# Performance work log

Measured on AMD Instinct MI355X. Metric: run time of the kernel, lower is better.

Reference implementation:

```python
import jax, jax.numpy as jnp
import numpy as np

EPS = 1e-5

def _lc(x, w, b, stride, pad):
    # x: [B,H,W]; w: [Ho,Wo,kh,kw]; b: [Ho,Wo]
    Ho, Wo, kh, kw = w.shape
    patches = jax.lax.conv_general_dilated_patches(
        x[:, None], (kh, kw), (stride, stride), [(pad, pad), (pad, pad)])
    # patches: [B, kh*kw, Ho, Wo]
    out = jnp.einsum('bkij,ijk->bij', patches, w.reshape(Ho, Wo, kh * kw))
    return out + b

def _ln2d(x, g, b):
    # torch LayerNorm over the last two (spatial) dims
    mu = x.mean(axis=(1, 2), keepdims=True)
    var = ((x - mu) ** 2).mean(axis=(1, 2), keepdims=True)
    return (x - mu) * jax.lax.rsqrt(var + EPS) * g + b

def _pool(x):
    # MaxPool2d(kernel=2, stride=2) over spatial dims of [B,H,W]
    return jax.lax.reduce_window(x, -jnp.inf, jax.lax.max, (1, 2, 2), (1, 2, 2), 'VALID')

def setup_inputs() -> dict:
    key = jax.random.key(0)
    ks = jax.random.split(key, 32)
    d = {}
    d['x'] = jax.random.normal(ks[0], (64, 128, 128), jnp.float32)
    sizes = [(128, 7), (64, 5), (64, 5), (32, 3), (32, 3), (16, 3)]
    for i, (s, k) in enumerate(sizes, start=1):
        d[f'w{i}'] = jax.random.normal(ks[4 * i], (s, s, k, k), jnp.float32) / k
        d[f'b{i}'] = jax.random.normal(ks[4 * i + 1], (s, s), jnp.float32)
        d[f'g{i}'] = jnp.ones((s, s), jnp.float32)
        d[f'be{i}'] = jnp.zeros((s, s), jnp.float32)
    d['fcw'] = jax.random.normal(ks[30], (1024, 256), jnp.float32) / np.sqrt(256.0)
    d['fcb'] = jax.random.normal(ks[31], (1024,), jnp.float32) * 0.01
    return d

def reference(x, w1, b1, g1, be1, w2, b2, g2, be2, w3, b3, g3, be3,
              w4, b4, g4, be4, w5, b5, g5, be5, w6, b6, g6, be6, fcw, fcb):
    # dropout is identity (eval / p=0)
    h = _pool(_ln2d(jax.nn.relu(_lc(x, w1, b1, 1, 3)), g1, be1))   # [B,64,64]
    h = _ln2d(jax.nn.relu(_lc(h, w2, b2, 1, 2)), g2, be2)          # [B,64,64]
    h = _pool(_ln2d(jax.nn.relu(_lc(h, w3, b3, 1, 2)), g3, be3))   # [B,32,32]
    h = _ln2d(jax.nn.relu(_lc(h, w4, b4, 1, 1)), g4, be4)          # [B,32,32]
    h = _pool(_ln2d(jax.nn.relu(_lc(h, w5, b5, 1, 1)), g5, be5))   # [B,16,16]
    h = _ln2d(jax.nn.relu(_lc(h, w6, b6, 1, 1)), g6, be6)          # [B,16,16]
    h = h.reshape(h.shape[0], -1) @ fcw.T + fcb                    # [B,1024]
    return jax.nn.softmax(h, axis=-1)
```

## Files before the change

### kernel.cpp

```cpp
#include <hip/hip_runtime.h>

#define LN_EPS 1e-5f

constexpr int T1_OFF   = 0;
constexpr int WT2_OFF  = 1048576;
constexpr int WT3_OFF  = WT2_OFF + 102400;
constexpr int WT4_OFF  = WT3_OFF + 102400;
constexpr int WT5_OFF  = WT4_OFF + 9216;
constexpr int WT6_OFF  = WT5_OFF + 9216;
constexpr int FCWT_OFF = WT6_OFF + 2304;

constexpr int NREP = 136;

__global__ __launch_bounds__(256) void s1_conv(const float* __restrict__ x,
                                               const float* __restrict__ w1,
                                               const float* __restrict__ b1,
                                               const float* __restrict__ w2,
                                               const float* __restrict__ w3,
                                               const float* __restrict__ w4,
                                               const float* __restrict__ w5,
                                               const float* __restrict__ w6,
                                               const float* __restrict__ fcw,
                                               float* __restrict__ ws)
{
    const int tid = threadIdx.x;

    if (blockIdx.x < NREP) {
        const int rb = blockIdx.x;
        if (rb < 32) {
            for (int idx = rb * 256 + tid; idx < 102400; idx += 32 * 256) {
                int p = idx / 25, k = idx % 25;
                ws[WT2_OFF + k * 4096 + p] = w2[idx];
            }
        } else if (rb < 64) {
            for (int idx = (rb - 32) * 256 + tid; idx < 102400; idx += 32 * 256) {
                int p = idx / 25, k = idx % 25;
                ws[WT3_OFF + k * 4096 + p] = w3[idx];
            }
        } else if (rb < 68) {
            for (int idx = (rb - 64) * 256 + tid; idx < 9216; idx += 4 * 256) {
                int p = idx / 9, k = idx % 9;
                ws[WT4_OFF + k * 1024 + p] = w4[idx];
            }
        } else if (rb < 72) {
            for (int idx = (rb - 68) * 256 + tid; idx < 9216; idx += 4 * 256) {
                int p = idx / 9, k = idx % 9;
                ws[WT5_OFF + k * 1024 + p] = w5[idx];
            }
        } else if (rb < 73) {
            for (int idx = tid; idx < 2304; idx += 256) {
                int p = idx / 9, k = idx % 9;
                ws[WT6_OFF + k * 256 + p] = w6[idx];
            }
        } else {
            for (int idx = (rb - 73) * 256 + tid; idx < 262144; idx += 63 * 256) {
                int r = idx >> 8, kc = idx & 255;
                int kq = kc >> 2, c = kc & 3;
                ws[FCWT_OFF + kq * 4096 + r * 4 + c] = fcw[idx];
            }
        }
        return;
    }

    constexpr int R = 128, K = 7, TILE = 8, S = 16, PAD = 3;
    constexpr int RT = TILE + K - 1;
    constexpr int PP = RT * RT + 1;
    constexpr int NBLK = R / TILE;
    constexpr int WCNT = TILE * TILE * K * K;
    constexpr int PG = 256 / S;
    constexpr int OPT = TILE * TILE / PG;

    __shared__ float s_in[S * PP];
    __shared__ float s_w[WCNT];
    __shared__ float s_b[TILE * TILE];

    float* t1 = ws + T1_OFF;
    const int cb = blockIdx.x - NREP;
    const int bt = cb % (NBLK * NBLK);
    const int sg = cb / (NBLK * NBLK);
    const int i0 = (bt / NBLK) * TILE;
    const int j0 = (bt % NBLK) * TILE;
    const int S0 = sg * S;

    for (int idx = tid; idx < WCNT; idx += 256) {
        int pi = idx / (K * K), kk = idx % (K * K);
        int gi = i0 + pi / TILE, gj = j0 + pi % TILE;
        s_w[idx] = w1[(gi * R + gj) * (K * K) + kk];
    }
    if (tid < TILE * TILE)
        s_b[tid] = b1[(i0 + tid / TILE) * R + (j0 + tid % TILE)];

    for (int idx = tid; idx < S * RT * RT; idx += 256) {
        int ls = idx / (RT * RT), p = idx % (RT * RT);
        int ci = i0 - PAD + p / RT, cj = j0 - PAD + p % RT;
        float v = 0.0f;
        if (ci >= 0 && ci < R && cj >= 0 && cj < R)
            v = x[(S0 + ls) * R * R + ci * R + cj];
        s_in[ls * PP + p] = v;
    }
    __syncthreads();

    const int s = tid % S;
    const int pg = tid / S;
    const int p0 = pg * OPT;
    const int ti = p0 / TILE, tj0 = p0 % TILE;
    float acc[OPT];
    #pragma unroll
    for (int o = 0; o < OPT; o++) acc[o] = s_b[p0 + o];
    #pragma unroll
    for (int ki = 0; ki < K; ki++) {
        float row[OPT + K - 1];
        #pragma unroll
        for (int c = 0; c < OPT + K - 1; c++)
            row[c] = s_in[s * PP + (ti + ki) * RT + tj0 + c];
        #pragma unroll
        for (int kj = 0; kj < K; kj++)
            #pragma unroll
            for (int o = 0; o < OPT; o++)
                acc[o] += row[o + kj] * s_w[(p0 + o) * (K * K) + ki * K + kj];
    }
    #pragma unroll
    for (int o = 0; o < OPT; o++)
        t1[(S0 + s) * R * R + (i0 + ti) * R + (j0 + tj0 + o)] = fmaxf(acc[o], 0.0f);
}

constexpr int NT = 1024;
constexpr int NW = NT / 64;

__device__ __forceinline__ void stats_reduce(float* red, float lsum, float lsq,
                                             float inv_n, float* s_mu, float* s_rs)
{
    const int tid = threadIdx.x;
    #pragma unroll
    for (int off = 32; off > 0; off >>= 1) {
        lsum += __shfl_down(lsum, off, 64);
        lsq  += __shfl_down(lsq,  off, 64);
    }
    if ((tid & 63) == 0) { red[tid >> 6] = lsum; red[NW + (tid >> 6)] = lsq; }
    __syncthreads();
    if (tid == 0) {
        float a = 0.f, b = 0.f;
        #pragma unroll
        for (int i = 0; i < NW; i++) { a += red[i]; b += red[NW + i]; }
        float mu = a * inv_n, ms = b * inv_n;
        *s_mu = mu;
        *s_rs = rsqrtf(ms - mu * mu + LN_EPS);
    }
    __syncthreads();
}

template<int M, int K>
__device__ __forceinline__ void conv_lds(const float* __restrict__ I,
                                         const float* __restrict__ wT,
                                         const float* __restrict__ bias,
                                         float* __restrict__ R,
                                         float& lsum, float& lsq)
{
    constexpr int NPOS = M * M;
    constexpr int PADK = (K - 1) / 2;
    constexpr int STR = M + 1;
    constexpr int OPT = (NPOS + NT - 1) / NT;
    const int tid = threadIdx.x;

    #pragma unroll
    for (int o = 0; o < OPT; o++) {
        int p = tid + o * NT;
        if (NPOS < NT && p >= NPOS) break;
        int i = p / M, j = p % M;
        float acc = bias[p];
        #pragma unroll
        for (int ki = 0; ki < K; ki++) {
            int ii = i - PADK + ki;
            bool rok = (ii >= 0 && ii < M);
            #pragma unroll
            for (int kj = 0; kj < K; kj++) {
                int jj = j - PADK + kj;
                float iv = (rok && jj >= 0 && jj < M) ? I[ii * STR + jj] : 0.0f;
                acc += iv * wT[(ki * K + kj) * NPOS + p];
            }
        }
        float v = fmaxf(acc, 0.0f);
        R[i * STR + j] = v;
        lsum += v;
        lsq  += v * v;
    }
}

template<int N, bool POOL>
__device__ __forceinline__ void transform(const float* __restrict__ R,
                                          float mu, float rs,
                                          const float* __restrict__ g,
                                          const float* __restrict__ b,
                                          float* __restrict__ I)
{
    constexpr int M = POOL ? N / 2 : N;
    constexpr int SR = N + 1, SI = M + 1;
    const int tid = threadIdx.x;
    for (int p = tid; p < M * M; p += NT) {
        int i = p / M, j = p % M;
        float v;
        if constexpr (POOL) {
            float best = -3.4e38f;
            #pragma unroll
            for (int dy = 0; dy < 2; dy++)
                #pragma unroll
                for (int dx = 0; dx < 2; dx++) {
                    int r = 2 * i + dy, c = 2 * j + dx;
                    float n = (R[r * SR + c] - mu) * rs * g[r * N + c] + b[r * N + c];
                    best = fmaxf(best, n);
                }
            v = best;
        } else {
            v = (R[i * SR + j] - mu) * rs * g[i * N + j] + b[i * N + j];
        }
        I[i * SI + j] = v;
    }
}

__global__ __launch_bounds__(1024) void tail_fused(
    const float* __restrict__ ws_ro,
    const float* __restrict__ g1, const float* __restrict__ be1,
    const float* __restrict__ b2,
    const float* __restrict__ g2, const float* __restrict__ be2,
    const float* __restrict__ b3,
    const float* __restrict__ g3, const float* __restrict__ be3,
    const float* __restrict__ b4,
    const float* __restrict__ g4, const float* __restrict__ be4,
    const float* __restrict__ b5,
    const float* __restrict__ g5, const float* __restrict__ be5,
    const float* __restrict__ b6,
    const float* __restrict__ g6, const float* __restrict__ be6,
    const float* __restrict__ fcb,
    float* __restrict__ outp)
{
    __shared__ __align__(16) float I[64 * 65];
    __shared__ __align__(16) float R[64 * 65];
    __shared__ __align__(16) float h[256];
    __shared__ float red[2 * NW];
    __shared__ float s_mu, s_rs;

    const int s = blockIdx.x;
    const int tid = threadIdx.x;
    const float* x1  = ws_ro + T1_OFF + s * 16384;
    const float* wT2 = ws_ro + WT2_OFF;
    const float* wT3 = ws_ro + WT3_OFF;
    const float* wT4 = ws_ro + WT4_OFF;
    const float* wT5 = ws_ro + WT5_OFF;
    const float* wT6 = ws_ro + WT6_OFF;

    float ls = 0.f, lq = 0.f;
    {
        const float4* x4 = (const float4*)x1;
        #pragma unroll
        for (int i = tid; i < 4096; i += NT) {
            float4 v = x4[i];
            ls += v.x + v.y + v.z + v.w;
            lq += v.x * v.x + v.y * v.y + v.z * v.z + v.w * v.w;
        }
    }
    stats_reduce(red, ls, lq, 1.f / 16384.f, &s_mu, &s_rs);

    {
        float mu = s_mu, rs = s_rs;
        #pragma unroll
        for (int o = 0; o < 4; o++) {
            int p = tid + o * NT;
            int i = p >> 6, j = p & 63;
            float2 xa = *((const float2*)(x1 + (2 * i) * 128 + 2 * j));
            float2 xb = *((const float2*)(x1 + (2 * i + 1) * 128 + 2 * j));
            float2 ga = *((const float2*)(g1 + (2 * i) * 128 + 2 * j));
            float2 gb = *((const float2*)(g1 + (2 * i + 1) * 128 + 2 * j));
            float2 ba = *((const float2*)(be1 + (2 * i) * 128 + 2 * j));
            float2 bb = *((const float2*)(be1 + (2 * i + 1) * 128 + 2 * j));
            float n0 = (xa.x - mu) * rs * ga.x + ba.x;
            float n1 = (xa.y - mu) * rs * ga.y + ba.y;
            float n2 = (xb.x - mu) * rs * gb.x + bb.x;
            float n3 = (xb.y - mu) * rs * gb.y + bb.y;
            I[i * 65 + j] = fmaxf(fmaxf(n0, n1), fmaxf(n2, n3));
        }
    }
    __syncthreads();

    ls = lq = 0.f; conv_lds<64, 5>(I, wT2, b2, R, ls, lq);
    stats_reduce(red, ls, lq, 1.f / 4096.f, &s_mu, &s_rs);
    transform<64, false>(R, s_mu, s_rs, g2, be2, I);
    __syncthreads();

    ls = lq = 0.f; conv_lds<64, 5>(I, wT3, b3, R, ls, lq);
    stats_reduce(red, ls, lq, 1.f / 4096.f, &s_mu, &s_rs);
    transform<64, true>(R, s_mu, s_rs, g3, be3, I);
    __syncthreads();

    ls = lq = 0.f; conv_lds<32, 3>(I, wT4, b4, R, ls, lq);
    stats_reduce(red, ls, lq, 1.f / 1024.f, &s_mu, &s_rs);
    transform<32, false>(R, s_mu, s_rs, g4, be4, I);
    __syncthreads();

    ls = lq = 0.f; conv_lds<32, 3>(I, wT5, b5, R, ls, lq);
    stats_reduce(red, ls, lq, 1.f / 1024.f, &s_mu, &s_rs);
    transform<32, true>(R, s_mu, s_rs, g5, be5, I);
    __syncthreads();

    ls = lq = 0.f; conv_lds<16, 3>(I, wT6, b6, R, ls, lq);
    stats_reduce(red, ls, lq, 1.f / 256.f, &s_mu, &s_rs);

    if (tid < 256) {
        int i = tid >> 4, j = tid & 15;
        h[tid] = (R[i * 17 + j] - s_mu) * s_rs * g6[tid] + be6[tid];
    }
    __syncthreads();

    float acc = fcb[tid];
    {
        const float4* wq = (const float4*)(ws_ro + FCWT_OFF);
        const float4* h4 = (const float4*)h;
        #pragma unroll 8
        for (int kq = 0; kq < 64; kq++) {
            float4 wv = wq[kq * 1024 + tid];
            float4 hv = h4[kq];
            acc += wv.x * hv.x + wv.y * hv.y + wv.z * hv.z + wv.w * hv.w;
        }
    }

    float m = acc;
    #pragma unroll
    for (int off = 32; off > 0; off >>= 1)
        m = fmaxf(m, __shfl_down(m, off, 64));
    if ((tid & 63) == 0) red[tid >> 6] = m;
    __syncthreads();
    if (tid == 0) {
        float mm = red[0];
        #pragma unroll
        for (int i = 1; i < NW; i++) mm = fmaxf(mm, red[i]);
        s_mu = mm;
    }
    __syncthreads();
    float e = expf(acc - s_mu);
    float sum = e;
    #pragma unroll
    for (int off = 32; off > 0; off >>= 1)
        sum += __shfl_down(sum, off, 64);
    if ((tid & 63) == 0) red[NW + (tid >> 6)] = sum;
    __syncthreads();
    if (tid == 0) {
        float ss = 0.f;
        #pragma unroll
        for (int i = 0; i < NW; i++) ss += red[NW + i];
        s_rs = 1.0f / ss;
    }
    __syncthreads();
    outp[s * 1024 + tid] = e * s_rs;
}

extern "C" void kernel_launch(void* const* d_in, const int* in_sizes, int n_in,
                              void* d_out, int out_size, void* d_ws, size_t ws_size,
                              hipStream_t stream) {
    (void)in_sizes; (void)n_in; (void)out_size; (void)ws_size;

    const float* x   = (const float*)d_in[0];
    const float* w1  = (const float*)d_in[1];  const float* b1  = (const float*)d_in[2];
    const float* g1  = (const float*)d_in[3];  const float* be1 = (const float*)d_in[4];
    const float* w2  = (const float*)d_in[5];  const float* b2  = (const float*)d_in[6];
    const float* g2  = (const float*)d_in[7];  const float* be2 = (const float*)d_in[8];
    const float* w3  = (const float*)d_in[9];  const float* b3  = (const float*)d_in[10];
    const float* g3  = (const float*)d_in[11]; const float* be3 = (const float*)d_in[12];
    const float* w4  = (const float*)d_in[13]; const float* b4  = (const float*)d_in[14];
    const float* g4  = (const float*)d_in[15]; const float* be4 = (const float*)d_in[16];
    const float* w5  = (const float*)d_in[17]; const float* b5  = (const float*)d_in[18];
    const float* g5  = (const float*)d_in[19]; const float* be5 = (const float*)d_in[20];
    const float* w6  = (const float*)d_in[21]; const float* b6  = (const float*)d_in[22];
    const float* g6  = (const float*)d_in[23]; const float* be6 = (const float*)d_in[24];
    const float* fcw = (const float*)d_in[25]; const float* fcb = (const float*)d_in[26];

    float* ws = (float*)d_ws;

    s1_conv<<<NREP + 1024, 256, 0, stream>>>(x, w1, b1, w2, w3, w4, w5, w6, fcw, ws);
    tail_fused<<<64, 1024, 0, stream>>>((const float*)ws,
        g1, be1, b2, g2, be2, b3, g3, be3,
        b4, g4, be4, b5, g5, be5, b6, g6, be6,
        fcb, (float*)d_out);
}
```

Before: 154.9 us.

## Register-block 64x64 5x5 convs and split FC+softmax into separate kernels

```diff
diff --git a/kernel.cpp b/kernel.cpp
--- a/kernel.cpp
+++ b/kernel.cpp
@@ -9,6 +9,8 @@
 constexpr int WT5_OFF  = WT4_OFF + 9216;
 constexpr int WT6_OFF  = WT5_OFF + 9216;
 constexpr int FCWT_OFF = WT6_OFF + 2304;
+constexpr int H_OFF    = FCWT_OFF + 262144;
+constexpr int LOG_OFF  = H_OFF + 16384;
 
 constexpr int NREP = 136;
 
@@ -149,6 +151,49 @@
     __syncthreads();
 }
 
+__device__ __forceinline__ void conv64_5cs(const float* __restrict__ I,
+                                           const float* __restrict__ wT,
+                                           const float* __restrict__ bias,
+                                           float* __restrict__ R,
+                                           float& lsum, float& lsq)
+{
+    const int tid = threadIdx.x;
+    const int j  = tid & 63;
+    const int rg = tid >> 6;
+    const int r0 = rg << 2;
+    float acc[4];
+    #pragma unroll
+    for (int r = 0; r < 4; r++) acc[r] = bias[(r0 + r) * 64 + j];
+
+    #pragma unroll
+    for (int dd = 0; dd < 8; dd++) {
+        const int ii = r0 - 2 + dd;
+        const bool rok = (ii >= 0 && ii < 64);
+        float c[5];
+        #pragma unroll
+        for (int kc = 0; kc < 5; kc++) {
+            int jj = j - 2 + kc;
+            c[kc] = (rok && jj >= 0 && jj < 64) ? I[ii * 65 + jj] : 0.f;
+        }
+        #pragma unroll
+        for (int r = 0; r < 4; r++) {
+            const int ki = dd - r;
+            if (ki >= 0 && ki < 5) {
+                #pragma unroll
+                for (int kj = 0; kj < 5; kj++)
+                    acc[r] += c[kj] * wT[(ki * 5 + kj) * 4096 + (r0 + r) * 64 + j];
+            }
+        }
+    }
+    #pragma unroll
+    for (int r = 0; r < 4; r++) {
+        float v = fmaxf(acc[r], 0.f);
+        R[(r0 + r) * 65 + j] = v;
+        lsum += v;
+        lsq  += v * v;
+    }
+}
+
 template<int M, int K>
 __device__ __forceinline__ void conv_lds(const float* __restrict__ I,
                                          const float* __restrict__ wT,
@@ -159,31 +204,25 @@
     constexpr int NPOS = M * M;
     constexpr int PADK = (K - 1) / 2;
     constexpr int STR = M + 1;
-    constexpr int OPT = (NPOS + NT - 1) / NT;
-    const int tid = threadIdx.x;
-
-    #pragma unroll
-    for (int o = 0; o < OPT; o++) {
-        int p = tid + o * NT;
-        if (NPOS < NT && p >= NPOS) break;
-        int i = p / M, j = p % M;
-        float acc = bias[p];
-        #pragma unroll
-        for (int ki = 0; ki < K; ki++) {
-            int ii = i - PADK + ki;
-            bool rok = (ii >= 0 && ii < M);
-            #pragma unroll
-            for (int kj = 0; kj < K; kj++) {
-                int jj = j - PADK + kj;
-                float iv = (rok && jj >= 0 && jj < M) ? I[ii * STR + jj] : 0.0f;
-                acc += iv * wT[(ki * K + kj) * NPOS + p];
-            }
-        }
-        float v = fmaxf(acc, 0.0f);
-        R[i * STR + j] = v;
-        lsum += v;
-        lsq  += v * v;
-    }
+    const int tid = threadIdx.x;
+    if (NPOS < NT && tid >= NPOS) return;
+    int i = tid / M, j = tid % M;
+    float acc = bias[tid];
+    #pragma unroll
+    for (int ki = 0; ki < K; ki++) {
+        int ii = i - PADK + ki;
+        bool rok = (ii >= 0 && ii < M);
+        #pragma unroll
+        for (int kj = 0; kj < K; kj++) {
+            int jj = j - PADK + kj;
+            float iv = (rok && jj >= 0 && jj < M) ? I[ii * STR + jj] : 0.0f;
+            acc += iv * wT[(ki * K + kj) * NPOS + tid];
+        }
+    }
+    float v = fmaxf(acc, 0.0f);
+    R[i * STR + j] = v;
+    lsum += v;
+    lsq  += v * v;
 }
 
 template<int N, bool POOL>
@@ -218,7 +257,7 @@
 }
 
 __global__ __launch_bounds__(1024) void tail_fused(
-    const float* __restrict__ ws_ro,
+    float* __restrict__ ws,
     const float* __restrict__ g1, const float* __restrict__ be1,
     const float* __restrict__ b2,
     const float* __restrict__ g2, const float* __restrict__ be2,
@@ -229,24 +268,21 @@
     const float* __restrict__ b5,
     const float* __restrict__ g5, const float* __restrict__ be5,
     const float* __restrict__ b6,
-    const float* __restrict__ g6, const float* __restrict__ be6,
-    const float* __restrict__ fcb,
-    float* __restrict__ outp)
+    const float* __restrict__ g6, const float* __restrict__ be6)
 {
     __shared__ __align__(16) float I[64 * 65];
     __shared__ __align__(16) float R[64 * 65];
-    __shared__ __align__(16) float h[256];
     __shared__ float red[2 * NW];
     __shared__ float s_mu, s_rs;
 
     const int s = blockIdx.x;
     const int tid = threadIdx.x;
-    const float* x1  = ws_ro + T1_OFF + s * 16384;
-    const float* wT2 = ws_ro + WT2_OFF;
-    const float* wT3 = ws_ro + WT3_OFF;
-    const float* wT4 = ws_ro + WT4_OFF;
-    const float* wT5 = ws_ro + WT5_OFF;
-    const float* wT6 = ws_ro + WT6_OFF;
+    const float* x1  = ws + T1_OFF + s * 16384;
+    const float* wT2 = ws + WT2_OFF;
+    const float* wT3 = ws + WT3_OFF;
+    const float* wT4 = ws + WT4_OFF;
+    const float* wT5 = ws + WT5_OFF;
+    const float* wT6 = ws + WT6_OFF;
 
     float ls = 0.f, lq = 0.f;
     {
@@ -281,12 +317,12 @@
     }
     __syncthreads();
 
-    ls = lq = 0.f; conv_lds<64, 5>(I, wT2, b2, R, ls, lq);
+    ls = lq = 0.f; conv64_5cs(I, wT2, b2, R, ls, lq);
     stats_reduce(red, ls, lq, 1.f / 4096.f, &s_mu, &s_rs);
     transform<64, false>(R, s_mu, s_rs, g2, be2, I);
     __syncthreads();
 
-    ls = lq = 0.f; conv_lds<64, 5>(I, wT3, b3, R, ls, lq);
+    ls = lq = 0.f; conv64_5cs(I, wT3, b3, R, ls, lq);
     stats_reduce(red, ls, lq, 1.f / 4096.f, &s_mu, &s_rs);
     transform<64, true>(R, s_mu, s_rs, g3, be3, I);
     __syncthreads();
@@ -306,50 +342,63 @@
 
     if (tid < 256) {
         int i = tid >> 4, j = tid & 15;
-        h[tid] = (R[i * 17 + j] - s_mu) * s_rs * g6[tid] + be6[tid];
-    }
-    __syncthreads();
-
-    float acc = fcb[tid];
-    {
-        const float4* wq = (const float4*)(ws_ro + FCWT_OFF);
-        const float4* h4 = (const float4*)h;
-        #pragma unroll 8
-        for (int kq = 0; kq < 64; kq++) {
-            float4 wv = wq[kq * 1024 + tid];
-            float4 hv = h4[kq];
-            acc += wv.x * hv.x + wv.y * hv.y + wv.z * hv.z + wv.w * hv.w;
-        }
-    }
-
-    float m = acc;
-    #pragma unroll
-    for (int off = 32; off > 0; off >>= 1)
-        m = fmaxf(m, __shfl_down(m, off, 64));
-    if ((tid & 63) == 0) red[tid >> 6] = m;
-    __syncthreads();
-    if (tid == 0) {
-        float mm = red[0];
-        #pragma unroll
-        for (int i = 1; i < NW; i++) mm = fmaxf(mm, red[i]);
-        s_mu = mm;
-    }
-    __syncthreads();
-    float e = expf(acc - s_mu);
-    float sum = e;
-    #pragma unroll
-    for (int off = 32; off > 0; off >>= 1)
-        sum += __shfl_down(sum, off, 64);
-    if ((tid & 63) == 0) red[NW + (tid >> 6)] = sum;
-    __syncthreads();
-    if (tid == 0) {
-        float ss = 0.f;
-        #pragma unroll
-        for (int i = 0; i < NW; i++) ss += red[NW + i];
-        s_rs = 1.0f / ss;
-    }
-    __syncthreads();
-    outp[s * 1024 + tid] = e * s_rs;
+        ws[H_OFF + s * 256 + tid] =
+            (R[i * 17 + j] - s_mu) * s_rs * g6[tid] + be6[tid];
+    }
+}
+
+__global__ __launch_bounds__(256) void fc_kernel(const float* __restrict__ ws_ro,
+                                                 const float* __restrict__ fcb,
+                                                 float* __restrict__ logits)
+{
+    __shared__ float h[256];
+    const int s = blockIdx.x >> 2, q = blockIdx.x & 3;
+    const int tid = threadIdx.x;
+    h[tid] = ws_ro[H_OFF + s * 256 + tid];
+    __syncthreads();
+    const int o = q * 256 + tid;
+    const float4* wq = (const float4*)(ws_ro + FCWT_OFF);
+    const float4* h4 = (const float4*)h;
+    float acc = fcb[o];
+    #pragma unroll 8
+    for (int kq = 0; kq < 64; kq++) {
+        float4 wv = wq[kq * 1024 + o];
+        float4 hv = h4[kq];
+        acc += wv.x * hv.x + wv.y * hv.y + wv.z * hv.z + wv.w * hv.w;
+    }
+    logits[s * 1024 + o] = acc;
+}
+
+__global__ __launch_bounds__(256) void softmax_k(const float* __restrict__ logits,
+                                                 float* __restrict__ out)
+{
+    __shared__ float red[256];
+    const int s = blockIdx.x;
+    const int tid = threadIdx.x;
+
+    float4 v = ((const float4*)(logits + s * 1024))[tid];
+    float lmax = fmaxf(fmaxf(v.x, v.y), fmaxf(v.z, v.w));
+    red[tid] = lmax;
+    __syncthreads();
+    for (int off = 128; off > 0; off >>= 1) {
+        if (tid < off) red[tid] = fmaxf(red[tid], red[tid + off]);
+        __syncthreads();
+    }
+    float M = red[0];
+    __syncthreads();
+
+    float4 e;
+    e.x = expf(v.x - M); e.y = expf(v.y - M);
+    e.z = expf(v.z - M); e.w = expf(v.w - M);
+    red[tid] = e.x + e.y + e.z + e.w;
+    __syncthreads();
+    for (int off = 128; off > 0; off >>= 1) {
+        if (tid < off) red[tid] += red[tid + off];
+        __syncthreads();
+    }
+    float inv = 1.0f / red[0];
+    e.x *= inv; e.y *= inv; e.z *= inv; e.w *= inv;
+    ((float4*)(out + s * 1024))[tid] = e;
 }
 
 extern "C" void kernel_launch(void* const* d_in, const int* in_sizes, int n_in,
@@ -375,8 +424,9 @@
     float* ws = (float*)d_ws;
 
     s1_conv<<<NREP + 1024, 256, 0, stream>>>(x, w1, b1, w2, w3, w4, w5, w6, fcw, ws);
-    tail_fused<<<64, 1024, 0, stream>>>((const float*)ws,
+    tail_fused<<<64, 1024, 0, stream>>>(ws,
         g1, be1, b2, g2, be2, b3, g3, be3,
-        b4, g4, be4, b5, g5, be5, b6, g6, be6,
-        fcb, (float*)d_out);
-}
+        b4, g4, be4, b5, g5, be5, b6, g6, be6);
+    fc_kernel<<<256, 256, 0, stream>>>((const float*)ws, fcb, ws + LOG_OFF);
+    softmax_k<<<64, 256, 0, stream>>>(ws + LOG_OFF, (float*)d_out);
+}
```

Result: slower. 180.6 us (+16.6%).
